# Performance work log

Measured on AMD Instinct MI355X. Metric: run time of the kernel, lower is better.

Reference implementation:

```python
import jax, jax.numpy as jnp
import numpy as np

T, B, D, H = 1024, 8, 1024, 16
HD = D // H  # head_dim = 64


def setup_inputs() -> dict:
    key = jax.random.key(0)
    ks = jax.random.split(key, 11)
    s = 1.0 / np.sqrt(D)
    return {
        "query": jax.random.normal(ks[0], (T, B, D), jnp.float32),
        "key": jax.random.normal(ks[1], (T, B, D), jnp.float32),
        "value": jax.random.normal(ks[2], (T, B, D), jnp.float32),
        "Wq": jax.random.normal(ks[3], (D, D), jnp.float32) * s,
        "bq": jax.random.normal(ks[4], (D,), jnp.float32) * s,
        "Wk": jax.random.normal(ks[5], (D, D), jnp.float32) * s,
        "bk": jax.random.normal(ks[6], (D,), jnp.float32) * s,
        "Wv": jax.random.normal(ks[7], (D, D), jnp.float32) * s,
        "bv": jax.random.normal(ks[8], (D,), jnp.float32) * s,
        "Wo": jax.random.normal(ks[9], (D, D), jnp.float32) * s,
        "bo": jax.random.normal(ks[10], (D,), jnp.float32) * s,
    }


def reference(query, key, value, Wq, bq, Wk, bk, Wv, bv, Wo, bo):
    # query/key/value: (T, B, D) seq-first, as in nn.MultiheadAttention
    t, b, d = query.shape
    scale = HD ** -0.5
    # projections (torch Linear: x @ W.T + b), split into heads -> (B, H, T, HD)
    q = (query @ Wq.T + bq).reshape(t, b, H, HD).transpose(1, 2, 0, 3)
    k = (key @ Wk.T + bk).reshape(t, b, H, HD).transpose(1, 2, 0, 3)
    v = (value @ Wv.T + bv).reshape(t, b, H, HD).transpose(1, 2, 0, 3)
    # full (B, H, T, T) scores, matching the module's explicit materialization
    attn = jnp.einsum('bhtd,bhsd->bhts', q, k) * scale
    attn = jax.nn.softmax(attn, axis=-1)
    # (B, H, T, HD) -> (T, B, D)
    out = jnp.einsum('bhts,bhsd->bhtd', attn, v)
    out = out.transpose(2, 0, 1, 3).reshape(t, b, d)
    return out @ Wo.T + bo
```

## Files before the change

kernel.cpp:

```cpp
#include <hip/hip_runtime.h>

#define T_SEQ 1024
#define BATCH 8
#define DMODEL 1024
#define NHEAD 16
#define HDIM 64
#define M_ROWS (T_SEQ * BATCH)
#define QSCALE (0.125f * 1.44269504088896f)

typedef unsigned short ushort_t;
typedef __attribute__((ext_vector_type(8))) short short8;
typedef __attribute__((ext_vector_type(4))) float f32x4;

#define G2L16(g, l) __builtin_amdgcn_global_load_lds(                      \
    (const __attribute__((address_space(1))) void*)(g),                    \
    (__attribute__((address_space(3))) void*)(l), 16, 0, 0)

static __device__ __forceinline__ ushort_t f2bf(float f) {
    unsigned int u = __builtin_bit_cast(unsigned int, f);
    u += 0x7FFFu + ((u >> 16) & 1u);
    return (ushort_t)(u >> 16);
}

#if __has_builtin(__builtin_amdgcn_cvt_pk_bf16_f32)
typedef __attribute__((ext_vector_type(2))) __bf16 bf16x2_t;
static __device__ __forceinline__ unsigned pk2(float lo, float hi) {
    bf16x2_t r = __builtin_amdgcn_cvt_pk_bf16_f32(lo, hi);
    return __builtin_bit_cast(unsigned, r);
}
#else
static __device__ __forceinline__ unsigned pk2(float lo, float hi) {
    return (unsigned)f2bf(lo) | ((unsigned)f2bf(hi) << 16);
}
#endif

#if __has_builtin(__builtin_amdgcn_exp2f)
#define EXP2F(x) __builtin_amdgcn_exp2f(x)
#else
#define EXP2F(x) exp2f(x)
#endif

__global__ __launch_bounds__(256) void cast3_bf16(
    const float4* __restrict__ a, const float4* __restrict__ b,
    const float4* __restrict__ c,
    uint2* __restrict__ oa, uint2* __restrict__ ob, uint2* __restrict__ oc,
    int n4)
{
    int i = blockIdx.x * 256 + threadIdx.x;
    if (i >= n4) return;
    const float4* src = (blockIdx.y == 0) ? a : (blockIdx.y == 1) ? b : c;
    uint2* dst        = (blockIdx.y == 0) ? oa : (blockIdx.y == 1) ? ob : oc;
    float4 v = src[i];
    uint2 o; o.x = pk2(v.x, v.y); o.y = pk2(v.z, v.w);
    dst[i] = o;
}

__global__ __launch_bounds__(256) void cast4_bf16(
    const float4* __restrict__ a, const float4* __restrict__ b,
    const float4* __restrict__ c, const float4* __restrict__ d,
    uint2* __restrict__ oa, uint2* __restrict__ ob,
    uint2* __restrict__ oc, uint2* __restrict__ od,
    int n4)
{
    int i = blockIdx.x * 256 + threadIdx.x;
    if (i >= n4) return;
    const float4* src = (blockIdx.y == 0) ? a : (blockIdx.y == 1) ? b
                      : (blockIdx.y == 2) ? c : d;
    uint2* dst        = (blockIdx.y == 0) ? oa : (blockIdx.y == 1) ? ob
                      : (blockIdx.y == 2) ? oc : od;
    float4 v = src[i];
    uint2 o; o.x = pk2(v.x, v.y); o.y = pk2(v.z, v.w);
    dst[i] = o;
}

template<bool OUT_BF16>
__global__ __launch_bounds__(256) void gemm_bt_mfma(
    const ushort_t* __restrict__ A, const ushort_t* __restrict__ Wbase,
    const float* __restrict__ bias0, const float* __restrict__ bias1,
    const float* __restrict__ bias2, void* __restrict__ Yv,
    int N, int K, float scale0)
{
    __shared__ ushort_t As[128 * 64];
    __shared__ ushort_t Bs[128 * 64];

    const int tid  = threadIdx.x;
    const int lane = tid & 63;
    const int quad = lane >> 4;
    const int l16  = lane & 15;
    const int w    = tid >> 6;
    const int wm   = w >> 1;
    const int wn   = w & 1;
    const int bn   = blockIdx.x;
    const int bmg  = blockIdx.y;

    const int sel = bmg >> 6;
    const ushort_t* Wb = Wbase + (size_t)sel * N * K;
    const float* bias = (sel == 0) ? bias0 : (sel == 1) ? bias1 : bias2;
    const float scale = (sel == 0) ? scale0 : 1.0f;

    const int srow_in = lane >> 3;
    const int sch     = lane & 7;

    const f32x4 zero4 = {0.f, 0.f, 0.f, 0.f};
    f32x4 acc[4][4];
#pragma unroll
    for (int i = 0; i < 4; i++)
#pragma unroll
        for (int j = 0; j < 4; j++) acc[i][j] = zero4;

    for (int k0 = 0; k0 < K; k0 += 64) {
        __syncthreads();
#pragma unroll
        for (int u = 0; u < 4; u++) {
            int seg = w * 4 + u;
            int row = seg * 8 + srow_in;
            int chs = sch ^ (row & 7);
            G2L16(&A [(size_t)(bmg * 128 + row) * K + k0 + chs * 8],
                  (char*)As + seg * 1024);
            G2L16(&Wb[(size_t)(bn  * 128 + row) * K + k0 + chs * 8],
                  (char*)Bs + seg * 1024);
        }
        __syncthreads();

#pragma unroll
        for (int ks = 0; ks < 2; ks++) {
            short8 af[4], bfr[4];
#pragma unroll
            for (int i = 0; i < 4; i++) {
                int row = wm * 64 + i * 16 + l16;
                af[i] = *(const short8*)&As[row * 64 + (((ks * 4 + quad) ^ (row & 7)) * 8)];
            }
#pragma unroll
            for (int j = 0; j < 4; j++) {
                int row = wn * 64 + j * 16 + l16;
                bfr[j] = *(const short8*)&Bs[row * 64 + (((ks * 4 + quad) ^ (row & 7)) * 8)];
            }
#pragma unroll
            for (int i = 0; i < 4; i++)
#pragma unroll
                for (int j = 0; j < 4; j++)
                    acc[i][j] = __builtin_amdgcn_mfma_f32_16x16x32_bf16(
                        af[i], bfr[j], acc[i][j], 0, 0, 0);
        }
    }

    float bj[4];
#pragma unroll
    for (int j = 0; j < 4; j++) bj[j] = bias[bn * 128 + wn * 64 + j * 16 + l16];
#pragma unroll
    for (int i = 0; i < 4; i++) {
#pragma unroll
        for (int r = 0; r < 4; r++) {
            size_t row = (size_t)(bmg * 128 + wm * 64 + i * 16 + quad * 4 + r);
#pragma unroll
            for (int j = 0; j < 4; j++) {
                int col = bn * 128 + wn * 64 + j * 16 + l16;
                float v = (acc[i][j][r] + bj[j]) * scale;
                if (OUT_BF16) ((ushort_t*)Yv)[row * N + col] = f2bf(v);
                else          ((float*)   Yv)[row * N + col] = v;
            }
        }
    }
}

__global__ __launch_bounds__(256) void transpose_v(
    const ushort_t* __restrict__ Vp, ushort_t* __restrict__ Vt)
{
    __shared__ ushort_t Ts[64][72];
    const int tid = threadIdx.x;
    const int t0 = blockIdx.x * 64;
    const int bh = blockIdx.y;
    const int b = bh >> 4, h = bh & 15;

#pragma unroll
    for (int u = 0; u < 2; u++) {
        int e = u * 256 + tid;
        int row = e >> 3, ch = (e & 7) * 8;
        uint4 v = *(const uint4*)&Vp[((size_t)(t0 + row) * BATCH + b) * DMODEL + h * 64 + ch];
        *(uint4*)&Ts[row][ch] = v;
    }
    __syncthreads();
#pragma unroll
    for (int u = 0; u < 2; u++) {
        int e = u * 256 + tid;
        int d = e >> 3, tc = (e & 7) * 8;
        uint4 o;
        o.x = (unsigned)Ts[tc + 0][d] | ((unsigned)Ts[tc + 1][d] << 16);
        o.y = (unsigned)Ts[tc + 2][d] | ((unsigned)Ts[tc + 3][d] << 16);
        o.z = (unsigned)Ts[tc + 4][d] | ((unsigned)Ts[tc + 5][d] << 16);
        o.w = (unsigned)Ts[tc + 6][d] | ((unsigned)Ts[tc + 7][d] << 16);
        *(uint4*)&Vt[((size_t)(bh * 64 + d)) * T_SEQ + t0 + tc] = o;
    }
}

__global__ __launch_bounds__(256) void attn_mfma(
    const ushort_t* __restrict__ Qp, const ushort_t* __restrict__ Kp,
    const ushort_t* __restrict__ VtG, ushort_t* __restrict__ Ao)
{
    __shared__ ushort_t Ks[64 * 64];
    __shared__ ushort_t Vs[64 * 64];
    __shared__ ushort_t Pl[4][32][72];

    const int tid  = threadIdx.x;
    const int lane = tid & 63;
    const int w    = tid >> 6;
    const int quad = lane >> 4;
    const int l16  = lane & 15;
    const int bid  = blockIdx.x;
    const int qb   = bid >> 7;
    const int bh   = bid & 127;
    const int b    = bh >> 4, h = bh & 15;
    const int hoff = h * 64;
    const int q0   = qb * 128 + w * 32;

    const int srow_in = lane >> 3;
    const int sch     = lane & 7;

    short8 qf[2][2];
#pragma unroll
    for (int rt = 0; rt < 2; rt++)
#pragma unroll
        for (int ks = 0; ks < 2; ks++)
            qf[rt][ks] = *(const short8*)&Qp[((size_t)(q0 + rt * 16 + l16) * BATCH + b) * DMODEL
                                             + hoff + ks * 32 + quad * 8];

    short8 ones;
#pragma unroll
    for (int i = 0; i < 8; i++) ones[i] = (short)0x3F80;

    const f32x4 zero4 = {0.f, 0.f, 0.f, 0.f};
    f32x4 oacc[2][4], lacc[2];
#pragma unroll
    for (int rt = 0; rt < 2; rt++) {
        lacc[rt] = zero4;
#pragma unroll
        for (int c = 0; c < 4; c++) oacc[rt][c] = zero4;
    }

    for (int s0 = 0; s0 < T_SEQ; s0 += 64) {
        __syncthreads();
#pragma unroll
        for (int u = 0; u < 2; u++) {
            int seg = w * 2 + u;
            int row = seg * 8 + srow_in;
            int chs = sch ^ (row & 7);
            G2L16(&Kp[((size_t)(s0 + row) * BATCH + b) * DMODEL + hoff + chs * 8],
                  (char*)Ks + seg * 1024);
            G2L16(&VtG[((size_t)(bh * 64 + row)) * T_SEQ + s0 + chs * 8],
                  (char*)Vs + seg * 1024);
        }
        __syncthreads();

        f32x4 sacc[2][4];
#pragma unroll
        for (int rt = 0; rt < 2; rt++)
#pragma unroll
            for (int c = 0; c < 4; c++) sacc[rt][c] = zero4;
#pragma unroll
        for (int c = 0; c < 4; c++) {
            int row = c * 16 + l16;
#pragma unroll
            for (int ks = 0; ks < 2; ks++) {
                short8 kf = *(const short8*)&Ks[row * 64 + (((ks * 4 + quad) ^ (row & 7)) * 8)];
#pragma unroll
                for (int rt = 0; rt < 2; rt++)
                    sacc[rt][c] = __builtin_amdgcn_mfma_f32_16x16x32_bf16(
                        kf, qf[rt][ks], sacc[rt][c], 0, 0, 0);
            }
        }

#pragma unroll
        for (int rt = 0; rt < 2; rt++)
#pragma unroll
            for (int c = 0; c < 4; c++) {
                uint2 pv;
                pv.x = pk2(EXP2F(sacc[rt][c][0]), EXP2F(sacc[rt][c][1]));
                pv.y = pk2(EXP2F(sacc[rt][c][2]), EXP2F(sacc[rt][c][3]));
                *(uint2*)&Pl[w][rt * 16 + l16][c * 16 + quad * 4] = pv;
            }

        short8 pf[2][2];
#pragma unroll
        for (int rt = 0; rt < 2; rt++)
#pragma unroll
            for (int ks = 0; ks < 2; ks++)
                pf[rt][ks] = *(const short8*)&Pl[w][rt * 16 + l16][ks * 32 + quad * 8];

#pragma unroll
        for (int rt = 0; rt < 2; rt++)
#pragma unroll
            for (int ks = 0; ks < 2; ks++)
                lacc[rt] = __builtin_amdgcn_mfma_f32_16x16x32_bf16(
                    ones, pf[rt][ks], lacc[rt], 0, 0, 0);

#pragma unroll
        for (int dt = 0; dt < 4; dt++) {
            int row = dt * 16 + l16;
#pragma unroll
            for (int ks = 0; ks < 2; ks++) {
                short8 vf = *(const short8*)&Vs[row * 64 + (((ks * 4 + quad) ^ (row & 7)) * 8)];
#pragma unroll
                for (int rt = 0; rt < 2; rt++)
                    oacc[rt][dt] = __builtin_amdgcn_mfma_f32_16x16x32_bf16(
                        vf, pf[rt][ks], oacc[rt][dt], 0, 0, 0);
            }
        }
    }

#pragma unroll
    for (int rt = 0; rt < 2; rt++) {
        float inv = 1.f / lacc[rt][0];
#pragma unroll
        for (int dt = 0; dt < 4; dt++) {
            uint2 ov;
            ov.x = pk2(oacc[rt][dt][0] * inv, oacc[rt][dt][1] * inv);
            ov.y = pk2(oacc[rt][dt][2] * inv, oacc[rt][dt][3] * inv);
            *(uint2*)&Pl[w][rt * 16 + l16][dt * 16 + quad * 4] = ov;
        }
    }
#pragma unroll
    for (int it = 0; it < 4; it++) {
        int row = it * 8 + (lane >> 3);
        int ch  = lane & 7;
        uint4 val = *(const uint4*)&Pl[w][row][ch * 8];
        *(uint4*)&Ao[((size_t)(q0 + row) * BATCH + b) * DMODEL + hoff + ch * 8] = val;
    }
}

extern "C" void kernel_launch(void* const* d_in, const int* in_sizes, int n_in,
                              void* d_out, int out_size, void* d_ws, size_t ws_size,
                              hipStream_t stream)
{
    const float* q  = (const float*)d_in[0];
    const float* k  = (const float*)d_in[1];
    const float* v  = (const float*)d_in[2];
    const float* Wq = (const float*)d_in[3];
    const float* bq = (const float*)d_in[4];
    const float* Wk = (const float*)d_in[5];
    const float* bk = (const float*)d_in[6];
    const float* Wv = (const float*)d_in[7];
    const float* bv = (const float*)d_in[8];
    const float* Wo = (const float*)d_in[9];
    const float* bo = (const float*)d_in[10];

    ushort_t* ws = (ushort_t*)d_ws;
    const size_t E = (size_t)M_ROWS * DMODEL;
    const size_t EW = (size_t)DMODEL * DMODEL;
    ushort_t* qb  = ws;
    ushort_t* kb  = ws + E;
    ushort_t* vb  = ws + 2 * E;
    ushort_t* Qp  = ws + 3 * E;
    ushort_t* Kp  = ws + 4 * E;
    ushort_t* Vp  = ws + 5 * E;
    ushort_t* Wqb = ws + 6 * E;
    ushort_t* Wkb = Wqb + EW;
    ushort_t* Wvb = Wkb + EW;
    ushort_t* Wob = Wvb + EW;
    ushort_t* Vt  = qb;
    ushort_t* Aob = kb;

    const int n4_in = (int)(E / 4);
    const int n4_w  = (int)(EW / 4);
    cast3_bf16<<<dim3(n4_in / 256, 3), 256, 0, stream>>>(
        (const float4*)q, (const float4*)k, (const float4*)v,
        (uint2*)qb, (uint2*)kb, (uint2*)vb, n4_in);
    cast4_bf16<<<dim3(n4_w / 256, 4), 256, 0, stream>>>(
        (const float4*)Wq, (const float4*)Wk, (const float4*)Wv, (const float4*)Wo,
        (uint2*)Wqb, (uint2*)Wkb, (uint2*)Wvb, (uint2*)Wob, n4_w);

    gemm_bt_mfma<true><<<dim3(DMODEL / 128, 3 * M_ROWS / 128), 256, 0, stream>>>(
        qb, Wqb, bq, bk, bv, Qp, DMODEL, DMODEL, QSCALE);

    transpose_v<<<dim3(T_SEQ / 64, BATCH * NHEAD), 256, 0, stream>>>(Vp, Vt);

    attn_mfma<<<dim3(8 * 128), 256, 0, stream>>>(Qp, Kp, Vt, Aob);

    gemm_bt_mfma<false><<<dim3(DMODEL / 128, M_ROWS / 128), 256, 0, stream>>>(
        Aob, Wob, bo, bo, bo, d_out, DMODEL, DMODEL, 1.0f);
}
```

Measured before the change: 336.6 us.

## Replace projection GEMMs with 256x256 double-buffered pipelined MFMA kernel and merge casts

The projection and output GEMMs move from 128x128 tiles with 256 threads and a single LDS buffer to 256x256 tiles with 512 threads. LDS is double-buffered and global-to-LDS loads are staged across four sub-phases, so loads overlap MFMA work. It also adds an XCD-aware block swizzle, setprio around MFMA bursts and explicit vmcnt waits. The two cast kernels become a single launch. The larger tiles raise register and LDS use to 128KB, cut occupancy, and leave fewer blocks (128 for the output GEMM) to fill the GPU.

```diff
diff --git a/kernel.cpp b/kernel.cpp
--- a/kernel.cpp
+++ b/kernel.cpp
@@ -16,6 +16,9 @@
     (const __attribute__((address_space(1))) void*)(g),                    \
     (__attribute__((address_space(3))) void*)(l), 16, 0, 0)
 
+#define SBAR()  __builtin_amdgcn_s_barrier()
+#define LGKM0() asm volatile("s_waitcnt lgkmcnt(0)" ::: "memory")
+
 static __device__ __forceinline__ ushort_t f2bf(float f) {
     unsigned int u = __builtin_bit_cast(unsigned int, f);
     u += 0x7FFFu + ((u >> 16) & 1u);
@@ -40,122 +43,216 @@
 #define EXP2F(x) exp2f(x)
 #endif
 
-__global__ __launch_bounds__(256) void cast3_bf16(
-    const float4* __restrict__ a, const float4* __restrict__ b,
-    const float4* __restrict__ c,
-    uint2* __restrict__ oa, uint2* __restrict__ ob, uint2* __restrict__ oc,
-    int n4)
+__global__ __launch_bounds__(256) void cast_all_bf16(
+    const float4* __restrict__ s0, const float4* __restrict__ s1,
+    const float4* __restrict__ s2, const float4* __restrict__ s3,
+    const float4* __restrict__ s4, const float4* __restrict__ s5,
+    const float4* __restrict__ s6,
+    uint2* __restrict__ d0, uint2* __restrict__ d1, uint2* __restrict__ d2,
+    uint2* __restrict__ d3, uint2* __restrict__ d4, uint2* __restrict__ d5,
+    uint2* __restrict__ d6, int n4big, int n4small)
 {
-    int i = blockIdx.x * 256 + threadIdx.x;
+    const int y = blockIdx.y;
+    const int n4 = (y < 3) ? n4big : n4small;
+    const int i = blockIdx.x * 256 + threadIdx.x;
     if (i >= n4) return;
-    const float4* src = (blockIdx.y == 0) ? a : (blockIdx.y == 1) ? b : c;
-    uint2* dst        = (blockIdx.y == 0) ? oa : (blockIdx.y == 1) ? ob : oc;
-    float4 v = src[i];
+    const float4* s; uint2* d;
+    switch (y) {
+        case 0: s = s0; d = d0; break;
+        case 1: s = s1; d = d1; break;
+        case 2: s = s2; d = d2; break;
+        case 3: s = s3; d = d3; break;
+        case 4: s = s4; d = d4; break;
+        case 5: s = s5; d = d5; break;
+        default: s = s6; d = d6; break;
+    }
+    float4 v = s[i];
     uint2 o; o.x = pk2(v.x, v.y); o.y = pk2(v.z, v.w);
-    dst[i] = o;
-}
-
-__global__ __launch_bounds__(256) void cast4_bf16(
-    const float4* __restrict__ a, const float4* __restrict__ b,
-    const float4* __restrict__ c, const float4* __restrict__ d,
-    uint2* __restrict__ oa, uint2* __restrict__ ob,
-    uint2* __restrict__ oc, uint2* __restrict__ od,
-    int n4)
-{
-    int i = blockIdx.x * 256 + threadIdx.x;
-    if (i >= n4) return;
-    const float4* src = (blockIdx.y == 0) ? a : (blockIdx.y == 1) ? b
-                      : (blockIdx.y == 2) ? c : d;
-    uint2* dst        = (blockIdx.y == 0) ? oa : (blockIdx.y == 1) ? ob
-                      : (blockIdx.y == 2) ? oc : od;
-    float4 v = src[i];
-    uint2 o; o.x = pk2(v.x, v.y); o.y = pk2(v.z, v.w);
-    dst[i] = o;
+    d[i] = o;
 }
 
 template<bool OUT_BF16>
-__global__ __launch_bounds__(256) void gemm_bt_mfma(
+__global__ __launch_bounds__(512) void gemm256_bt(
     const ushort_t* __restrict__ A, const ushort_t* __restrict__ Wbase,
     const float* __restrict__ bias0, const float* __restrict__ bias1,
     const float* __restrict__ bias2, void* __restrict__ Yv,
     int N, int K, float scale0)
 {
-    __shared__ ushort_t As[128 * 64];
-    __shared__ ushort_t Bs[128 * 64];
+    __shared__ ushort_t As[2][256 * 64];
+    __shared__ ushort_t Bs[2][256 * 64];
 
     const int tid  = threadIdx.x;
     const int lane = tid & 63;
+    const int w    = tid >> 6;
+    const int wm   = w >> 2;
+    const int wn   = w & 3;
     const int quad = lane >> 4;
     const int l16  = lane & 15;
-    const int w    = tid >> 6;
-    const int wm   = w >> 1;
-    const int wn   = w & 1;
-    const int bn   = blockIdx.x;
-    const int bmg  = blockIdx.y;
-
-    const int sel = bmg >> 6;
+    const int srow = lane >> 3;
+    const int sch  = lane & 7;
+
+    const int nwg = gridDim.x * gridDim.y;
+    const int lin = blockIdx.y * gridDim.x + blockIdx.x;
+    const int qq  = nwg >> 3;
+    const int swz = (lin & 7) * qq + (lin >> 3);
+    const int bn  = swz & 3;
+    const int bmg = swz >> 2;
+
+    const int sel = bmg >> 5;
     const ushort_t* Wb = Wbase + (size_t)sel * N * K;
     const float* bias = (sel == 0) ? bias0 : (sel == 1) ? bias1 : bias2;
     const float scale = (sel == 0) ? scale0 : 1.0f;
 
-    const int srow_in = lane >> 3;
-    const int sch     = lane & 7;
+    const size_t arow0 = (size_t)bmg * 256;
+    const size_t brow0 = (size_t)bn * 256;
+    const int scol = (sch ^ srow) * 8;
+
+    size_t aoff[2][2], boff[2][2];
+#pragma unroll
+    for (int h = 0; h < 2; h++)
+#pragma unroll
+        for (int u = 0; u < 2; u++) {
+            const int rl = h * 128 + (w * 2 + u) * 8 + srow;
+            aoff[h][u] = (arow0 + rl) * (size_t)K + scol;
+            boff[h][u] = (brow0 + rl) * (size_t)K + scol;
+        }
+
+    const int c0 = (quad ^ (l16 & 7)) * 8;
+    const int c1 = c0 ^ 32;
 
     const f32x4 zero4 = {0.f, 0.f, 0.f, 0.f};
-    f32x4 acc[4][4];
-#pragma unroll
-    for (int i = 0; i < 4; i++)
+    f32x4 acc[8][4];
+#pragma unroll
+    for (int i = 0; i < 8; i++)
 #pragma unroll
         for (int j = 0; j < 4; j++) acc[i][j] = zero4;
 
-    for (int k0 = 0; k0 < K; k0 += 64) {
-        __syncthreads();
-#pragma unroll
-        for (int u = 0; u < 4; u++) {
-            int seg = w * 4 + u;
-            int row = seg * 8 + srow_in;
-            int chs = sch ^ (row & 7);
-            G2L16(&A [(size_t)(bmg * 128 + row) * K + k0 + chs * 8],
-                  (char*)As + seg * 1024);
-            G2L16(&Wb[(size_t)(bn  * 128 + row) * K + k0 + chs * 8],
-                  (char*)Bs + seg * 1024);
-        }
-        __syncthreads();
-
-#pragma unroll
-        for (int ks = 0; ks < 2; ks++) {
-            short8 af[4], bfr[4];
-#pragma unroll
-            for (int i = 0; i < 4; i++) {
-                int row = wm * 64 + i * 16 + l16;
-                af[i] = *(const short8*)&As[row * 64 + (((ks * 4 + quad) ^ (row & 7)) * 8)];
-            }
+    short8 af[4][2];
+    short8 bfx[2][2][2];
+
+    const int nT = K >> 6;
+
+#define STAGE_A(t, buf, h)                                                  \
+    do {                                                                    \
+        G2L16(A + aoff[h][0] + (t) * 64,                                    \
+              (char*)&As[buf][0] + (h) * 16384 + (w * 2 + 0) * 1024);       \
+        G2L16(A + aoff[h][1] + (t) * 64,                                    \
+              (char*)&As[buf][0] + (h) * 16384 + (w * 2 + 1) * 1024);       \
+    } while (0)
+#define STAGE_B(t, buf, h)                                                  \
+    do {                                                                    \
+        G2L16(Wb + boff[h][0] + (t) * 64,                                   \
+              (char*)&Bs[buf][0] + (h) * 16384 + (w * 2 + 0) * 1024);       \
+        G2L16(Wb + boff[h][1] + (t) * 64,                                   \
+              (char*)&Bs[buf][0] + (h) * 16384 + (w * 2 + 1) * 1024);       \
+    } while (0)
+
+    STAGE_A(0, 0, 0); STAGE_A(0, 0, 1);
+    STAGE_B(0, 0, 0); STAGE_B(0, 0, 1);
+    STAGE_B(1, 1, 0); STAGE_B(1, 1, 1);
+    asm volatile("s_waitcnt vmcnt(4)" ::: "memory");
+    SBAR();
+
+    for (int kt = 0; kt < nT; ++kt) {
+        const int cur = kt & 1;
+
+        if (kt + 1 < nT) STAGE_A(kt + 1, cur ^ 1, 0);
+#pragma unroll
+        for (int ii = 0; ii < 4; ii++) {
+            const int row = wm * 128 + ii * 16 + l16;
+            af[ii][0] = *(const short8*)&As[cur][row * 64 + c0];
+            af[ii][1] = *(const short8*)&As[cur][row * 64 + c1];
+        }
+#pragma unroll
+        for (int jj = 0; jj < 2; jj++) {
+            const int row = wn * 64 + jj * 16 + l16;
+            bfx[0][jj][0] = *(const short8*)&Bs[cur][row * 64 + c0];
+            bfx[0][jj][1] = *(const short8*)&Bs[cur][row * 64 + c1];
+        }
+        __builtin_amdgcn_s_setprio(1);
+#pragma unroll
+        for (int ii = 0; ii < 4; ii++)
+#pragma unroll
+            for (int jj = 0; jj < 2; jj++)
+#pragma unroll
+                for (int ks = 0; ks < 2; ks++)
+                    acc[ii][jj] = __builtin_amdgcn_mfma_f32_16x16x32_bf16(
+                        af[ii][ks], bfx[0][jj][ks], acc[ii][jj], 0, 0, 0);
+        __builtin_amdgcn_s_setprio(0);
+        LGKM0();
+        SBAR();
+
+        if (kt + 1 < nT) STAGE_A(kt + 1, cur ^ 1, 1);
+#pragma unroll
+        for (int jj = 0; jj < 2; jj++) {
+            const int row = wn * 64 + 32 + jj * 16 + l16;
+            bfx[1][jj][0] = *(const short8*)&Bs[cur][row * 64 + c0];
+            bfx[1][jj][1] = *(const short8*)&Bs[cur][row * 64 + c1];
+        }
+        __builtin_amdgcn_s_setprio(1);
+#pragma unroll
+        for (int ii = 0; ii < 4; ii++)
+#pragma unroll
+            for (int jj = 0; jj < 2; jj++)
+#pragma unroll
+                for (int ks = 0; ks < 2; ks++)
+                    acc[ii][2 + jj] = __builtin_amdgcn_mfma_f32_16x16x32_bf16(
+                        af[ii][ks], bfx[1][jj][ks], acc[ii][2 + jj], 0, 0, 0);
+        __builtin_amdgcn_s_setprio(0);
+        LGKM0();
+        SBAR();
+
+        if (kt + 2 < nT) STAGE_B(kt + 2, cur, 0);
+#pragma unroll
+        for (int ii = 0; ii < 4; ii++) {
+            const int row = wm * 128 + 64 + ii * 16 + l16;
+            af[ii][0] = *(const short8*)&As[cur][row * 64 + c0];
+            af[ii][1] = *(const short8*)&As[cur][row * 64 + c1];
+        }
+        __builtin_amdgcn_s_setprio(1);
+#pragma unroll
+        for (int ii = 0; ii < 4; ii++)
+#pragma unroll
+            for (int jj = 0; jj < 2; jj++)
+#pragma unroll
+                for (int ks = 0; ks < 2; ks++)
+                    acc[4 + ii][jj] = __builtin_amdgcn_mfma_f32_16x16x32_bf16(
+                        af[ii][ks], bfx[0][jj][ks], acc[4 + ii][jj], 0, 0, 0);
+        __builtin_amdgcn_s_setprio(0);
+        LGKM0();
+        SBAR();
+
+        if (kt + 2 < nT) STAGE_B(kt + 2, cur, 1);
+        __builtin_amdgcn_s_setprio(1);
+#pragma unroll
+        for (int ii = 0; ii < 4; ii++)
+#pragma unroll
+            for (int jj = 0; jj < 2; jj++)
+#pragma unroll
+                for (int ks = 0; ks < 2; ks++)
+                    acc[4 + ii][2 + jj] = __builtin_amdgcn_mfma_f32_16x16x32_bf16(
+                        af[ii][ks], bfx[1][jj][ks], acc[4 + ii][2 + jj], 0, 0, 0);
+        __builtin_amdgcn_s_setprio(0);
+        LGKM0();
+        if (kt < nT - 2) asm volatile("s_waitcnt vmcnt(4)" ::: "memory");
+        else             asm volatile("s_waitcnt vmcnt(0)" ::: "memory");
+        SBAR();
+    }
+#undef STAGE_A
+#undef STAGE_B
+
+    float bj[4];
+#pragma unroll
+    for (int j = 0; j < 4; j++) bj[j] = bias[bn * 256 + wn * 64 + j * 16 + l16];
+#pragma unroll
+    for (int il = 0; il < 8; il++) {
+#pragma unroll
+        for (int r = 0; r < 4; r++) {
+            const size_t row = (size_t)bmg * 256 + wm * 128 + il * 16 + quad * 4 + r;
 #pragma unroll
             for (int j = 0; j < 4; j++) {
-                int row = wn * 64 + j * 16 + l16;
-                bfr[j] = *(const short8*)&Bs[row * 64 + (((ks * 4 + quad) ^ (row & 7)) * 8)];
-            }
-#pragma unroll
-            for (int i = 0; i < 4; i++)
-#pragma unroll
-                for (int j = 0; j < 4; j++)
-                    acc[i][j] = __builtin_amdgcn_mfma_f32_16x16x32_bf16(
-                        af[i], bfr[j], acc[i][j], 0, 0, 0);
-        }
-    }
-
-    float bj[4];
-#pragma unroll
-    for (int j = 0; j < 4; j++) bj[j] = bias[bn * 128 + wn * 64 + j * 16 + l16];
-#pragma unroll
-    for (int i = 0; i < 4; i++) {
-#pragma unroll
-        for (int r = 0; r < 4; r++) {
-            size_t row = (size_t)(bmg * 128 + wm * 64 + i * 16 + quad * 4 + r);
-#pragma unroll
-            for (int j = 0; j < 4; j++) {
-                int col = bn * 128 + wn * 64 + j * 16 + l16;
-                float v = (acc[i][j][r] + bj[j]) * scale;
+                const int col = bn * 256 + wn * 64 + j * 16 + l16;
+                const float v = (acc[il][j][r] + bj[j]) * scale;
                 if (OUT_BF16) ((ushort_t*)Yv)[row * N + col] = f2bf(v);
                 else          ((float*)   Yv)[row * N + col] = v;
             }
@@ -361,20 +458,20 @@
 
     const int n4_in = (int)(E / 4);
     const int n4_w  = (int)(EW / 4);
-    cast3_bf16<<<dim3(n4_in / 256, 3), 256, 0, stream>>>(
+    cast_all_bf16<<<dim3(n4_in / 256, 7), 256, 0, stream>>>(
         (const float4*)q, (const float4*)k, (const float4*)v,
-        (uint2*)qb, (uint2*)kb, (uint2*)vb, n4_in);
-    cast4_bf16<<<dim3(n4_w / 256, 4), 256, 0, stream>>>(
         (const float4*)Wq, (const float4*)Wk, (const float4*)Wv, (const float4*)Wo,
-        (uint2*)Wqb, (uint2*)Wkb, (uint2*)Wvb, (uint2*)Wob, n4_w);
-
-    gemm_bt_mfma<true><<<dim3(DMODEL / 128, 3 * M_ROWS / 128), 256, 0, stream>>>(
+        (uint2*)qb, (uint2*)kb, (uint2*)vb,
+        (uint2*)Wqb, (uint2*)Wkb, (uint2*)Wvb, (uint2*)Wob,
+        n4_in, n4_w);
+
+    gemm256_bt<true><<<dim3(DMODEL / 256, 3 * M_ROWS / 256), 512, 0, stream>>>(
         qb, Wqb, bq, bk, bv, Qp, DMODEL, DMODEL, QSCALE);
 
     transpose_v<<<dim3(T_SEQ / 64, BATCH * NHEAD), 256, 0, stream>>>(Vp, Vt);
 
     attn_mfma<<<dim3(8 * 128), 256, 0, stream>>>(Qp, Kp, Vt, Aob);
 
-    gemm_bt_mfma<false><<<dim3(DMODEL / 128, M_ROWS / 128), 256, 0, stream>>>(
+    gemm256_bt<false><<<dim3(DMODEL / 256, M_ROWS / 256), 512, 0, stream>>>(
         Aob, Wob, bo, bo, bo, d_out, DMODEL, DMODEL, 1.0f);
 }
```

After: 352.4 us. 1.05x slower.
